# Performance work log

Hardware: AMD Instinct MI355X
Metric: run time of the kernel (lower is better)

## Reference

```python
import jax, jax.numpy as jnp
import numpy as np

FREQ_RES = 100.0 / 256.0
NUM_FILTERS = 6
_CFG = [(0.5, 4.0), (4.0, 8.0), (8.0, 12.0), (12.0, 16.0), (16.0, 24.0), (24.0, 30.0)]
BANDS = [(int(a / FREQ_RES), int(b / FREQ_RES)) for a, b in _CFG]  # (start_bin, end_bin)


def _interp_idx(n_src, n_dst):
    # torch F.interpolate bilinear, align_corners=False, along last dim (T dim is identity since same size)
    j = np.arange(n_dst)
    src = np.maximum((j + 0.5) * n_src / n_dst - 0.5, 0.0)
    x0 = np.floor(src).astype(np.int32)
    x1 = np.minimum(x0 + 1, n_src - 1)
    w = (src - x0).astype(np.float32)
    return x0, x1, w


def _gelu(x):
    return jax.nn.gelu(x, approximate=False)


def _forward(spec, centers, widths, gains, align_w, align_b, fc1_w, fc1_b, fc2_w, fc2_b,
             band_gain, gate_w, gate_b, proj_w, proj_b, bn_gamma, bn_beta, bn_mean, bn_var):
    B, C, T, F = spec.shape
    N = NUM_FILTERS
    band_feats = []
    for i, (s, e) in enumerate(BANDS):
        nb = e - s + 1
        sl = spec[:, :, :, s:e + 1]                       # [B,C,T,nb]
        mu = jax.nn.softplus(centers[i]) + s              # [C,N]
        mu = jnp.clip(mu, s, s + nb - 1)
        std = jnp.clip(jax.nn.softplus(widths[i]) + 1e-3, 0.5, 2.0 * nb / N)
        freqs = jnp.arange(nb, dtype=spec.dtype)          # relative bins [nb]
        g = jnp.exp(-0.5 * ((freqs[None, None, :] - mu[:, :, None]) / std[:, :, None]) ** 2)  # [C,N,nb]
        w = gains[i][:, :, None] * g / (g.sum(-1, keepdims=True) + 1e-6)
        filt = jnp.einsum('bctf,cnf->bctn', sl, w)        # [B,C,T,N]
        aligned = jnp.einsum('bctn,dc->bdtn', filt, align_w[i]) + align_b[i][None, :, None, None]
        band_feats.append(aligned)
    band_stack = jnp.stack(band_feats, axis=1)            # [B,6,C,T,N]
    nb_bands = band_stack.shape[1]
    x = band_stack.reshape(B, nb_bands * C, T, N)
    h = _gelu(jnp.einsum('bktn,ok->botn', x, fc1_w) + fc1_b[None, :, None, None])
    attn = jnp.einsum('botn,ko->bktn', h, fc2_w) + fc2_b[None, :, None, None]
    attn = jax.nn.softmax(attn.reshape(B, nb_bands, C, T, N), axis=1)  # softmax over bands
    band_stack = band_stack * attn * band_gain[None, :, None, None, None]
    enhanced = jnp.zeros_like(spec)
    for i, (s, e) in enumerate(BANDS):
        nb = e - s + 1
        narrow = band_stack[:, i]                         # [B,C,T,N]
        x0, x1, wl = _interp_idx(NUM_FILTERS, nb)
        wl = jnp.asarray(wl, dtype=spec.dtype)
        bf = narrow[..., x0] * (1.0 - wl) + narrow[..., x1] * wl   # [B,C,T,nb]
        enhanced = enhanced.at[:, :, :, s:e + 1].add(bf)
    residual = enhanced - spec
    gate = jax.nn.sigmoid(jnp.einsum('bctf,dc->bdtf', residual, gate_w) + gate_b[None, :, None, None])
    enhanced2 = spec + gate * residual
    y = jnp.einsum('bctf,dc->bdtf', enhanced2, proj_w) + proj_b[None, :, None, None]
    y = (y - bn_mean[None, :, None, None]) / jnp.sqrt(bn_var[None, :, None, None] + 1e-5)
    y = y * bn_gamma[None, :, None, None] + bn_beta[None, :, None, None]
    return _gelu(y)


def setup_inputs() -> dict:
    key = jax.random.key(0)
    ks = jax.random.split(key, 8)
    B, C, T, F, N = 64, 3, 3000, 103, NUM_FILTERS
    spec = jax.random.normal(ks[0], (B, C, T, F), dtype=jnp.float32)
    centers = jnp.stack([jnp.broadcast_to(jnp.linspace(a, b, N, dtype=jnp.float32) / FREQ_RES, (C, N)) for a, b in _CFG])
    widths = jnp.stack([jnp.full((C, N), (b - a) / N / FREQ_RES, dtype=jnp.float32) for a, b in _CFG])
    gains = jnp.ones((6, C, N), jnp.float32)
    align_w = jax.random.normal(ks[1], (6, C, C), dtype=jnp.float32) / np.sqrt(C)
    align_b = jax.random.normal(ks[2], (6, C), dtype=jnp.float32) * 0.02
    inter = 2 * C
    fc1_w = jax.random.normal(ks[3], (inter, 6 * C), dtype=jnp.float32) / np.sqrt(6 * C)
    fc1_b = jnp.zeros((inter,), jnp.float32)
    fc2_w = jax.random.normal(ks[4], (6 * C, inter), dtype=jnp.float32) / np.sqrt(inter)
    fc2_b = jnp.zeros((6 * C,), jnp.float32)
    band_gain = jnp.ones((6,), jnp.float32)
    gate_w = jax.random.normal(ks[5], (C, C), dtype=jnp.float32) / np.sqrt(C)
    gate_b = jnp.zeros((C,), jnp.float32)
    proj_w = jax.random.normal(ks[6], (C, C), dtype=jnp.float32) / np.sqrt(C)
    proj_b = jnp.zeros((C,), jnp.float32)
    bn_gamma = jnp.ones((C,), jnp.float32)
    bn_beta = jnp.zeros((C,), jnp.float32)
    bn_mean = jnp.zeros((C,), jnp.float32)
    bn_var = jnp.ones((C,), jnp.float32)
    return {"spec": spec, "centers": centers, "widths": widths, "gains": gains,
            "align_w": align_w, "align_b": align_b, "fc1_w": fc1_w, "fc1_b": fc1_b,
            "fc2_w": fc2_w, "fc2_b": fc2_b, "band_gain": band_gain,
            "gate_w": gate_w, "gate_b": gate_b, "proj_w": proj_w, "proj_b": proj_b,
            "bn_gamma": bn_gamma, "bn_beta": bn_beta, "bn_mean": bn_mean, "bn_var": bn_var}


def reference(spec, centers, widths, gains, align_w, align_b, fc1_w, fc1_b, fc2_w, fc2_b,
              band_gain, gate_w, gate_b, proj_w, proj_b, bn_gamma, bn_beta, bn_mean, bn_var):
    return _forward(spec, centers, widths, gains, align_w, align_b, fc1_w, fc1_b, fc2_w, fc2_b,
                    band_gain, gate_w, gate_b, proj_w, proj_b, bn_gamma, bn_beta, bn_mean, bn_var)
```

## Files before the change

### kernel.cpp

```cpp
#include <hip/hip_runtime.h>
#include <math.h>

namespace {

constexpr int C_ = 3, T_ = 3000, F_ = 103, NB_ = 6;
constexpr int TT = 12;
constexpr int BS[NB_]  = {1, 10, 20, 30, 40, 61};
constexpr int BNB[NB_] = {10, 11, 11, 11, 22, 16};
constexpr int BOF[NB_] = {0, 10, 21, 32, 43, 65};
constexpr int SPF = 81;
constexpr int PLANE = T_ * F_;
constexpr int SEC = TT * F_;
constexpr int WTOT = 81 * 18;
constexpr int POOLN = C_ * TT * SPF + WTOT;

__device__ __forceinline__ float softplus_full_(float x) {
  return fmaxf(x, 0.0f) + log1pf(expf(-fabsf(x)));
}
__device__ __forceinline__ float sigmoid_(float z) {
  return 1.0f / (1.0f + __expf(-z));
}
__device__ __forceinline__ float gelu_(float x) {
  return x * sigmoid_(1.595769122f * x * (1.0f + 0.044715f * x * x));
}

__global__ __launch_bounds__(128)
void prep_kernel(const float* __restrict__ centers,
                 const float* __restrict__ widths,
                 const float* __restrict__ gains,
                 float* __restrict__ wfilt)
{
  const int q = threadIdx.x;
  if (q >= 108) return;
  int i = q / 18;
  int p = q - i * 18;
  int s = BS[i], nb = BNB[i];
  float mu = softplus_full_(centers[q]) + (float)s;
  mu = fminf(fmaxf(mu, (float)s), (float)(s + nb - 1));
  float sd = softplus_full_(widths[q]) + 0.001f;
  sd = fminf(fmaxf(sd, 0.5f), 2.0f * (float)nb / 6.0f);
  float sum = 0.0f;
  for (int f = 0; f < nb; ++f) {
    float d = ((float)f - mu) / sd;
    sum += __expf(-0.5f * d * d);
  }
  float sc = gains[q] / (sum + 1e-6f);
  float* wrow = &wfilt[BOF[i] * 18 + p * nb];
  for (int f = 0; f < nb; ++f) {
    float d = ((float)f - mu) / sd;
    wrow[f] = sc * __expf(-0.5f * d * d);
  }
}

__global__ __launch_bounds__(256, 6)
void sleepband_kernel(const float* __restrict__ spec,
                      const float* __restrict__ wfilt,
                      const float* __restrict__ align_w,
                      const float* __restrict__ align_b,
                      const float* __restrict__ fc1_w,
                      const float* __restrict__ fc1_b,
                      const float* __restrict__ fc2_w,
                      const float* __restrict__ fc2_b,
                      const float* __restrict__ band_gain,
                      const float* __restrict__ gate_w,
                      const float* __restrict__ gate_b,
                      const float* __restrict__ proj_w,
                      const float* __restrict__ proj_b,
                      const float* __restrict__ bn_gamma,
                      const float* __restrict__ bn_beta,
                      const float* __restrict__ bn_mean,
                      const float* __restrict__ bn_var,
                      float* __restrict__ out)
{
  __shared__ __align__(16) float sPool[POOLN];
  __shared__ float sBand[TT][109];
  __shared__ float sAw[54], sAb[18], sF1[108], sF1b[6], sF2[108], sF2b[18],
                   sBg[6], sGw[9], sGb[3], sPw[9], sPb[3];

  const int tid = threadIdx.x;
  const int t0  = blockIdx.x * TT;
  const int b   = blockIdx.y;

  float* sW = sPool + C_ * TT * SPF;

  const float* specB = spec + (size_t)b * C_ * PLANE;
  for (int li = tid; li < C_ * TT * SPF; li += 256) {
    int c   = li / (TT * SPF);
    int rem = li - c * (TT * SPF);
    int tt  = rem / SPF;
    int f   = rem - tt * SPF;
    sPool[li] = specB[(size_t)c * PLANE + (size_t)(t0 + tt) * F_ + f];
  }
  for (int k = tid; k < WTOT; k += 256) sW[k] = wfilt[k];

  if (tid < 54)  sAw[tid]  = align_w[tid];
  if (tid < 18)  sAb[tid]  = align_b[tid];
  if (tid < 108) sF1[tid]  = fc1_w[tid];
  if (tid < 6)   sF1b[tid] = fc1_b[tid];
  if (tid < 108) sF2[tid]  = fc2_w[tid];
  if (tid < 18)  sF2b[tid] = fc2_b[tid];
  if (tid < 6)   sBg[tid]  = band_gain[tid];
  if (tid < 9)   sGw[tid]  = gate_w[tid];
  if (tid < 3)   sGb[tid]  = gate_b[tid];
  if (tid < 9) {
    int d = tid / 3;
    float sc = bn_gamma[d] * __frsqrt_rn(bn_var[d] + 1e-5f);
    sPw[tid] = proj_w[tid] * sc;
  }
  if (tid < 3) {
    float sc = bn_gamma[tid] * __frsqrt_rn(bn_var[tid] + 1e-5f);
    sPb[tid] = (proj_b[tid] - bn_mean[tid]) * sc + bn_beta[tid];
  }
  __syncthreads();

  if (tid < 18 * TT) {
    int p  = tid / TT;
    int tt = tid - p * TT;
    int c  = p / 6;
    int n  = p - c * 6;
    const float* srowb = &sPool[(c * TT + tt) * SPF];
    #pragma unroll
    for (int i = 0; i < NB_; ++i) {
      const float* wrow = &sW[BOF[i] * 18 + p * BNB[i]];
      const float* srow = srowb + BS[i];
      float acc = 0.0f;
      #pragma unroll
      for (int f = 0; f < BNB[i]; ++f) acc += srow[f] * wrow[f];
      sBand[tt][(i * 3 + c) * 6 + n] = acc;
    }
  }
  __syncthreads();

  if (tid < 6 * TT) {
    int n  = tid / TT;
    int tt = tid - n * TT;
    float al[18];
    #pragma unroll
    for (int i = 0; i < 6; ++i) {
      float f0 = sBand[tt][(i * 3 + 0) * 6 + n];
      float f1 = sBand[tt][(i * 3 + 1) * 6 + n];
      float f2 = sBand[tt][(i * 3 + 2) * 6 + n];
      #pragma unroll
      for (int d = 0; d < 3; ++d)
        al[i * 3 + d] = sAw[i * 9 + d * 3 + 0] * f0 + sAw[i * 9 + d * 3 + 1] * f1 +
                        sAw[i * 9 + d * 3 + 2] * f2 + sAb[i * 3 + d];
    }
    float h[6];
    #pragma unroll
    for (int o = 0; o < 6; ++o) {
      float acc = sF1b[o];
      #pragma unroll
      for (int k = 0; k < 18; ++k) acc += sF1[o * 18 + k] * al[k];
      h[o] = gelu_(acc);
    }
    float at[18];
    #pragma unroll
    for (int k = 0; k < 18; ++k) {
      float acc = sF2b[k];
      #pragma unroll
      for (int o = 0; o < 6; ++o) acc += sF2[k * 6 + o] * h[o];
      at[k] = acc;
    }
    #pragma unroll
    for (int c = 0; c < 3; ++c) {
      float m = at[c];
      #pragma unroll
      for (int i = 1; i < 6; ++i) m = fmaxf(m, at[i * 3 + c]);
      float e[6], ssum = 0.0f;
      #pragma unroll
      for (int i = 0; i < 6; ++i) { e[i] = __expf(at[i * 3 + c] - m); ssum += e[i]; }
      float inv = 1.0f / ssum;
      #pragma unroll
      for (int i = 0; i < 6; ++i)
        sBand[tt][(i * 3 + c) * 6 + n] = al[i * 3 + c] * (e[i] * inv) * sBg[i];
    }
  }
  __syncthreads();

  if (tid < C_ * TT) {
    const int c  = tid / TT;
    const int tt = tid - c * TT;
    float bnd[36];
    #pragma unroll
    for (int i = 0; i < 6; ++i)
      #pragma unroll
      for (int n = 0; n < 6; ++n)
        bnd[i * 6 + n] = sBand[tt][(i * 3 + c) * 6 + n];
    float* row = &sPool[c * SEC + tt * F_];
    row[0] = 0.0f;
    float carry = 0.0f;
    #pragma unroll
    for (int i = 0; i < NB_; ++i) {
      #pragma unroll
      for (int j = 0; j < BNB[i]; ++j) {
        float src = ((float)j + 0.5f) * 6.0f / (float)BNB[i] - 0.5f;
        src = src > 0.0f ? src : 0.0f;
        int   x0 = (int)src;
        int   x1 = (x0 < 5) ? x0 + 1 : 5;
        float wl = src - (float)x0;
        float v  = bnd[i * 6 + x0] * (1.0f - wl) + bnd[i * 6 + x1] * wl;
        if (j == 0) v += carry;
        if (i < NB_ - 1 && j == BNB[i] - 1) carry = v;
        else row[BS[i] + j] = v;
      }
    }
    #pragma unroll
    for (int f = 77; f < F_; ++f) row[f] = 0.0f;
  }
  __syncthreads();

  float gw[9], pw[9], gb3[3], pb3[3];
  #pragma unroll
  for (int k = 0; k < 9; ++k) { gw[k] = sGw[k]; pw[k] = sPw[k]; }
  #pragma unroll
  for (int k = 0; k < 3; ++k) { gb3[k] = sGb[k]; pb3[k] = sPb[k]; }

  const float* sp0 = specB + (size_t)t0 * F_;
  float* outB = out + (size_t)b * C_ * PLANE + (size_t)t0 * F_;
  for (int e4 = tid; e4 < SEC / 4; e4 += 256) {
    const int e = e4 * 4;
    const float4 sA = *(const float4*)(sp0 + e);
    const float4 sB = *(const float4*)(sp0 + PLANE + e);
    const float4 sC = *(const float4*)(sp0 + 2 * PLANE + e);
    const float4 eA = *(const float4*)&sPool[0 * SEC + e];
    const float4 eB = *(const float4*)&sPool[1 * SEC + e];
    const float4 eC = *(const float4*)&sPool[2 * SEC + e];
    float4 oA, oB, oC;
    const float* sAp = (const float*)&sA; const float* sBp = (const float*)&sB;
    const float* sCp = (const float*)&sC;
    const float* eAp = (const float*)&eA; const float* eBp = (const float*)&eB;
    const float* eCp = (const float*)&eC;
    float* oAp = (float*)&oA; float* oBp = (float*)&oB; float* oCp = (float*)&oC;
    #pragma unroll
    for (int j = 0; j < 4; ++j) {
      float sv0 = sAp[j], sv1 = sBp[j], sv2 = sCp[j];
      float r0 = eAp[j] - sv0, r1 = eBp[j] - sv1, r2 = eCp[j] - sv2;
      float e20 = sv0 + sigmoid_(gw[0] * r0 + gw[1] * r1 + gw[2] * r2 + gb3[0]) * r0;
      float e21 = sv1 + sigmoid_(gw[3] * r0 + gw[4] * r1 + gw[5] * r2 + gb3[1]) * r1;
      float e22 = sv2 + sigmoid_(gw[6] * r0 + gw[7] * r1 + gw[8] * r2 + gb3[2]) * r2;
      float y0 = pw[0] * e20 + pw[1] * e21 + pw[2] * e22 + pb3[0];
      float y1 = pw[3] * e20 + pw[4] * e21 + pw[5] * e22 + pb3[1];
      float y2 = pw[6] * e20 + pw[7] * e21 + pw[8] * e22 + pb3[2];
      oAp[j] = gelu_(y0); oBp[j] = gelu_(y1); oCp[j] = gelu_(y2);
    }
    *(float4*)(outB + e) = oA;
    *(float4*)(outB + PLANE + e) = oB;
    *(float4*)(outB + 2 * PLANE + e) = oC;
  }
}

}

extern "C" void kernel_launch(void* const* d_in, const int* in_sizes, int n_in,
                              void* d_out, int out_size, void* d_ws, size_t ws_size,
                              hipStream_t stream) {
  (void)n_in; (void)out_size; (void)ws_size;
  const int B = in_sizes[0] / (C_ * T_ * F_);
  float* wfilt = (float*)d_ws;
  prep_kernel<<<1, 128, 0, stream>>>(
      (const float*)d_in[1], (const float*)d_in[2], (const float*)d_in[3], wfilt);
  dim3 grid(T_ / TT, B);
  sleepband_kernel<<<grid, 256, 0, stream>>>(
      (const float*)d_in[0],  wfilt,
      (const float*)d_in[4],  (const float*)d_in[5],
      (const float*)d_in[6],  (const float*)d_in[7],  (const float*)d_in[8],
      (const float*)d_in[9],  (const float*)d_in[10], (const float*)d_in[11],
      (const float*)d_in[12], (const float*)d_in[13], (const float*)d_in[14],
      (const float*)d_in[15], (const float*)d_in[16], (const float*)d_in[17],
      (const float*)d_in[18], (float*)d_out);
}
```

Baseline: 279.6 us.

## Pad band slots for float4 filter dots, enlarge time tile, hoist BN fold

Spectrum bins are staged into shared memory in a padded per-band slot layout, and filter weights are zero-padded to multiples of four so each band dot product runs as float4 loads. The time tile grows from 12 to 20 rows and the block from 256 to 384 threads. The BN fold into proj weights moves into the prep kernel. Small MLP and gate parameters are now read directly from global memory instead of being staged in shared memory. Larger tiles raise shared memory per block and may cut occupancy, and the direct global reads of uniform weights rely on the cache.

```diff
diff --git a/kernel.cpp b/kernel.cpp
--- a/kernel.cpp
+++ b/kernel.cpp
@@ -4,15 +4,21 @@
 namespace {
 
 constexpr int C_ = 3, T_ = 3000, F_ = 103, NB_ = 6;
-constexpr int TT = 12;
-constexpr int BS[NB_]  = {1, 10, 20, 30, 40, 61};
-constexpr int BNB[NB_] = {10, 11, 11, 11, 22, 16};
-constexpr int BOF[NB_] = {0, 10, 21, 32, 43, 65};
-constexpr int SPF = 81;
+constexpr int TT = 20;
+constexpr int BS_[NB_]  = {1, 10, 20, 30, 40, 61};
+constexpr int BNB_[NB_] = {10, 11, 11, 11, 22, 16};
+constexpr int BP_[NB_]  = {12, 12, 12, 12, 24, 16};
+constexpr int BPS_[NB_] = {0, 12, 24, 36, 48, 72};
+constexpr int WOFP_[NB_] = {0, 216, 432, 648, 864, 1296};
+constexpr int WTOTP = 1584;
+constexpr int SLOTS = 88;
+constexpr int CTSTR = 92;
+constexpr int SPECN = C_ * TT * CTSTR;
 constexpr int PLANE = T_ * F_;
-constexpr int SEC = TT * F_;
-constexpr int WTOT = 81 * 18;
-constexpr int POOLN = C_ * TT * SPF + WTOT;
+constexpr int SEC  = TT * F_;
+constexpr int SECP = 2064;
+constexpr int POOLN = SPECN + WTOTP;
+constexpr int NTHR = 384;
 
 __device__ __forceinline__ float softplus_full_(float x) {
   return fmaxf(x, 0.0f) + log1pf(expf(-fabsf(x)));
@@ -28,33 +34,49 @@
 void prep_kernel(const float* __restrict__ centers,
                  const float* __restrict__ widths,
                  const float* __restrict__ gains,
-                 float* __restrict__ wfilt)
+                 const float* __restrict__ proj_w,
+                 const float* __restrict__ proj_b,
+                 const float* __restrict__ bn_gamma,
+                 const float* __restrict__ bn_beta,
+                 const float* __restrict__ bn_mean,
+                 const float* __restrict__ bn_var,
+                 float* __restrict__ ws)
 {
   const int q = threadIdx.x;
-  if (q >= 108) return;
-  int i = q / 18;
-  int p = q - i * 18;
-  int s = BS[i], nb = BNB[i];
-  float mu = softplus_full_(centers[q]) + (float)s;
-  mu = fminf(fmaxf(mu, (float)s), (float)(s + nb - 1));
-  float sd = softplus_full_(widths[q]) + 0.001f;
-  sd = fminf(fmaxf(sd, 0.5f), 2.0f * (float)nb / 6.0f);
-  float sum = 0.0f;
-  for (int f = 0; f < nb; ++f) {
-    float d = ((float)f - mu) / sd;
-    sum += __expf(-0.5f * d * d);
-  }
-  float sc = gains[q] / (sum + 1e-6f);
-  float* wrow = &wfilt[BOF[i] * 18 + p * nb];
-  for (int f = 0; f < nb; ++f) {
-    float d = ((float)f - mu) / sd;
-    wrow[f] = sc * __expf(-0.5f * d * d);
-  }
-}
-
-__global__ __launch_bounds__(256, 6)
+  if (q < 108) {
+    int i = q / 18;
+    int p = q - i * 18;
+    int s = BS_[i], nb = BNB_[i];
+    float mu = softplus_full_(centers[q]) + (float)s;
+    mu = fminf(fmaxf(mu, (float)s), (float)(s + nb - 1));
+    float sd = softplus_full_(widths[q]) + 0.001f;
+    sd = fminf(fmaxf(sd, 0.5f), 2.0f * (float)nb / 6.0f);
+    float sum = 0.0f;
+    for (int f = 0; f < nb; ++f) {
+      float d = ((float)f - mu) / sd;
+      sum += __expf(-0.5f * d * d);
+    }
+    float sc = gains[q] / (sum + 1e-6f);
+    float* wrow = &ws[WOFP_[i] + p * BP_[i]];
+    for (int f = 0; f < nb; ++f) {
+      float d = ((float)f - mu) / sd;
+      wrow[f] = sc * __expf(-0.5f * d * d);
+    }
+    for (int f = nb; f < BP_[i]; ++f) wrow[f] = 0.0f;
+  } else if (q < 117) {
+    int k = q - 108, d = k / 3;
+    float sc = bn_gamma[d] / sqrtf(bn_var[d] + 1e-5f);
+    ws[WTOTP + k] = proj_w[k] * sc;
+  } else if (q < 120) {
+    int d = q - 117;
+    float sc = bn_gamma[d] / sqrtf(bn_var[d] + 1e-5f);
+    ws[WTOTP + 9 + d] = (proj_b[d] - bn_mean[d]) * sc + bn_beta[d];
+  }
+}
+
+__global__ __launch_bounds__(NTHR, 6)
 void sleepband_kernel(const float* __restrict__ spec,
-                      const float* __restrict__ wfilt,
+                      const float* __restrict__ ws,
                       const float* __restrict__ align_w,
                       const float* __restrict__ align_b,
                       const float* __restrict__ fc1_w,
@@ -64,76 +86,57 @@
                       const float* __restrict__ band_gain,
                       const float* __restrict__ gate_w,
                       const float* __restrict__ gate_b,
-                      const float* __restrict__ proj_w,
-                      const float* __restrict__ proj_b,
-                      const float* __restrict__ bn_gamma,
-                      const float* __restrict__ bn_beta,
-                      const float* __restrict__ bn_mean,
-                      const float* __restrict__ bn_var,
                       float* __restrict__ out)
 {
   __shared__ __align__(16) float sPool[POOLN];
   __shared__ float sBand[TT][109];
-  __shared__ float sAw[54], sAb[18], sF1[108], sF1b[6], sF2[108], sF2b[18],
-                   sBg[6], sGw[9], sGb[3], sPw[9], sPb[3];
 
   const int tid = threadIdx.x;
   const int t0  = blockIdx.x * TT;
   const int b   = blockIdx.y;
-
-  float* sW = sPool + C_ * TT * SPF;
-
   const float* specB = spec + (size_t)b * C_ * PLANE;
-  for (int li = tid; li < C_ * TT * SPF; li += 256) {
-    int c   = li / (TT * SPF);
-    int rem = li - c * (TT * SPF);
-    int tt  = rem / SPF;
-    int f   = rem - tt * SPF;
-    sPool[li] = specB[(size_t)c * PLANE + (size_t)(t0 + tt) * F_ + f];
-  }
-  for (int k = tid; k < WTOT; k += 256) sW[k] = wfilt[k];
-
-  if (tid < 54)  sAw[tid]  = align_w[tid];
-  if (tid < 18)  sAb[tid]  = align_b[tid];
-  if (tid < 108) sF1[tid]  = fc1_w[tid];
-  if (tid < 6)   sF1b[tid] = fc1_b[tid];
-  if (tid < 108) sF2[tid]  = fc2_w[tid];
-  if (tid < 18)  sF2b[tid] = fc2_b[tid];
-  if (tid < 6)   sBg[tid]  = band_gain[tid];
-  if (tid < 9)   sGw[tid]  = gate_w[tid];
-  if (tid < 3)   sGb[tid]  = gate_b[tid];
-  if (tid < 9) {
-    int d = tid / 3;
-    float sc = bn_gamma[d] * __frsqrt_rn(bn_var[d] + 1e-5f);
-    sPw[tid] = proj_w[tid] * sc;
-  }
-  if (tid < 3) {
-    float sc = bn_gamma[tid] * __frsqrt_rn(bn_var[tid] + 1e-5f);
-    sPb[tid] = (proj_b[tid] - bn_mean[tid]) * sc + bn_beta[tid];
-  }
+
+  for (int li = tid; li < C_ * TT * SLOTS; li += NTHR) {
+    int ctt  = li / SLOTS;
+    int slot = li - ctt * SLOTS;
+    int c    = ctt / TT;
+    int tt   = ctt - c * TT;
+    int i    = (slot >= 72) ? 5 : ((slot >= 48) ? 4 : (slot / 12));
+    int j    = slot - BPS_[i];
+    float v  = 0.0f;
+    if (j < BNB_[i])
+      v = specB[(size_t)c * PLANE + (size_t)(t0 + tt) * F_ + (BS_[i] + j)];
+    sPool[ctt * CTSTR + slot] = v;
+  }
+  for (int k = tid; k < WTOTP; k += NTHR) sPool[SPECN + k] = ws[k];
   __syncthreads();
 
   if (tid < 18 * TT) {
-    int p  = tid / TT;
-    int tt = tid - p * TT;
-    int c  = p / 6;
-    int n  = p - c * 6;
-    const float* srowb = &sPool[(c * TT + tt) * SPF];
+    const int p  = tid / TT;
+    const int tt = tid - p * TT;
+    const int c  = p / 6;
+    const int n  = p - c * 6;
+    const float* srow = &sPool[(c * TT + tt) * CTSTR];
+    const float* wall = &sPool[SPECN];
     #pragma unroll
     for (int i = 0; i < NB_; ++i) {
-      const float* wrow = &sW[BOF[i] * 18 + p * BNB[i]];
-      const float* srow = srowb + BS[i];
-      float acc = 0.0f;
-      #pragma unroll
-      for (int f = 0; f < BNB[i]; ++f) acc += srow[f] * wrow[f];
-      sBand[tt][(i * 3 + c) * 6 + n] = acc;
+      const float4* s4 = (const float4*)(srow + BPS_[i]);
+      const float4* w4 = (const float4*)(wall + WOFP_[i] + p * BP_[i]);
+      float4 a = {0.0f, 0.0f, 0.0f, 0.0f};
+      #pragma unroll
+      for (int k = 0; k < BP_[i] / 4; ++k) {
+        float4 sv = s4[k], wv = w4[k];
+        a.x += sv.x * wv.x; a.y += sv.y * wv.y;
+        a.z += sv.z * wv.z; a.w += sv.w * wv.w;
+      }
+      sBand[tt][(i * 3 + c) * 6 + n] = (a.x + a.y) + (a.z + a.w);
     }
   }
   __syncthreads();
 
   if (tid < 6 * TT) {
-    int n  = tid / TT;
-    int tt = tid - n * TT;
+    const int n  = tid / TT;
+    const int tt = tid - n * TT;
     float al[18];
     #pragma unroll
     for (int i = 0; i < 6; ++i) {
@@ -142,23 +145,23 @@
       float f2 = sBand[tt][(i * 3 + 2) * 6 + n];
       #pragma unroll
       for (int d = 0; d < 3; ++d)
-        al[i * 3 + d] = sAw[i * 9 + d * 3 + 0] * f0 + sAw[i * 9 + d * 3 + 1] * f1 +
-                        sAw[i * 9 + d * 3 + 2] * f2 + sAb[i * 3 + d];
+        al[i * 3 + d] = align_w[i * 9 + d * 3 + 0] * f0 + align_w[i * 9 + d * 3 + 1] * f1 +
+                        align_w[i * 9 + d * 3 + 2] * f2 + align_b[i * 3 + d];
     }
     float h[6];
     #pragma unroll
     for (int o = 0; o < 6; ++o) {
-      float acc = sF1b[o];
-      #pragma unroll
-      for (int k = 0; k < 18; ++k) acc += sF1[o * 18 + k] * al[k];
+      float acc = fc1_b[o];
+      #pragma unroll
+      for (int k = 0; k < 18; ++k) acc += fc1_w[o * 18 + k] * al[k];
       h[o] = gelu_(acc);
     }
     float at[18];
     #pragma unroll
     for (int k = 0; k < 18; ++k) {
-      float acc = sF2b[k];
-      #pragma unroll
-      for (int o = 0; o < 6; ++o) acc += sF2[k * 6 + o] * h[o];
+      float acc = fc2_b[k];
+      #pragma unroll
+      for (int o = 0; o < 6; ++o) acc += fc2_w[k * 6 + o] * h[o];
       at[k] = acc;
     }
     #pragma unroll
@@ -172,7 +175,7 @@
       float inv = 1.0f / ssum;
       #pragma unroll
       for (int i = 0; i < 6; ++i)
-        sBand[tt][(i * 3 + c) * 6 + n] = al[i * 3 + c] * (e[i] * inv) * sBg[i];
+        sBand[tt][(i * 3 + c) * 6 + n] = al[i * 3 + c] * (e[i] * inv) * band_gain[i];
     }
   }
   __syncthreads();
@@ -186,22 +189,22 @@
       #pragma unroll
       for (int n = 0; n < 6; ++n)
         bnd[i * 6 + n] = sBand[tt][(i * 3 + c) * 6 + n];
-    float* row = &sPool[c * SEC + tt * F_];
+    float* row = &sPool[c * SECP + tt * F_];
     row[0] = 0.0f;
     float carry = 0.0f;
     #pragma unroll
     for (int i = 0; i < NB_; ++i) {
       #pragma unroll
-      for (int j = 0; j < BNB[i]; ++j) {
-        float src = ((float)j + 0.5f) * 6.0f / (float)BNB[i] - 0.5f;
+      for (int j = 0; j < BNB_[i]; ++j) {
+        float src = ((float)j + 0.5f) * 6.0f / (float)BNB_[i] - 0.5f;
         src = src > 0.0f ? src : 0.0f;
         int   x0 = (int)src;
         int   x1 = (x0 < 5) ? x0 + 1 : 5;
         float wl = src - (float)x0;
         float v  = bnd[i * 6 + x0] * (1.0f - wl) + bnd[i * 6 + x1] * wl;
         if (j == 0) v += carry;
-        if (i < NB_ - 1 && j == BNB[i] - 1) carry = v;
-        else row[BS[i] + j] = v;
+        if (i < NB_ - 1 && j == BNB_[i] - 1) carry = v;
+        else row[BS_[i] + j] = v;
       }
     }
     #pragma unroll
@@ -211,20 +214,20 @@
 
   float gw[9], pw[9], gb3[3], pb3[3];
   #pragma unroll
-  for (int k = 0; k < 9; ++k) { gw[k] = sGw[k]; pw[k] = sPw[k]; }
+  for (int k = 0; k < 9; ++k) { gw[k] = gate_w[k]; pw[k] = ws[WTOTP + k]; }
   #pragma unroll
-  for (int k = 0; k < 3; ++k) { gb3[k] = sGb[k]; pb3[k] = sPb[k]; }
+  for (int k = 0; k < 3; ++k) { gb3[k] = gate_b[k]; pb3[k] = ws[WTOTP + 9 + k]; }
 
   const float* sp0 = specB + (size_t)t0 * F_;
   float* outB = out + (size_t)b * C_ * PLANE + (size_t)t0 * F_;
-  for (int e4 = tid; e4 < SEC / 4; e4 += 256) {
+  for (int e4 = tid; e4 < SEC / 4; e4 += NTHR) {
     const int e = e4 * 4;
     const float4 sA = *(const float4*)(sp0 + e);
     const float4 sB = *(const float4*)(sp0 + PLANE + e);
     const float4 sC = *(const float4*)(sp0 + 2 * PLANE + e);
-    const float4 eA = *(const float4*)&sPool[0 * SEC + e];
-    const float4 eB = *(const float4*)&sPool[1 * SEC + e];
-    const float4 eC = *(const float4*)&sPool[2 * SEC + e];
+    const float4 eA = *(const float4*)&sPool[0 * SECP + e];
+    const float4 eB = *(const float4*)&sPool[1 * SECP + e];
+    const float4 eC = *(const float4*)&sPool[2 * SECP + e];
     float4 oA, oB, oC;
     const float* sAp = (const float*)&sA; const float* sBp = (const float*)&sB;
     const float* sCp = (const float*)&sC;
@@ -256,16 +259,16 @@
                               hipStream_t stream) {
   (void)n_in; (void)out_size; (void)ws_size;
   const int B = in_sizes[0] / (C_ * T_ * F_);
-  float* wfilt = (float*)d_ws;
+  float* ws = (float*)d_ws;
   prep_kernel<<<1, 128, 0, stream>>>(
-      (const float*)d_in[1], (const float*)d_in[2], (const float*)d_in[3], wfilt);
+      (const float*)d_in[1],  (const float*)d_in[2],  (const float*)d_in[3],
+      (const float*)d_in[13], (const float*)d_in[14], (const float*)d_in[15],
+      (const float*)d_in[16], (const float*)d_in[17], (const float*)d_in[18], ws);
   dim3 grid(T_ / TT, B);
-  sleepband_kernel<<<grid, 256, 0, stream>>>(
-      (const float*)d_in[0],  wfilt,
+  sleepband_kernel<<<grid, NTHR, 0, stream>>>(
+      (const float*)d_in[0],  ws,
       (const float*)d_in[4],  (const float*)d_in[5],
       (const float*)d_in[6],  (const float*)d_in[7],  (const float*)d_in[8],
       (const float*)d_in[9],  (const float*)d_in[10], (const float*)d_in[11],
-      (const float*)d_in[12], (const float*)d_in[13], (const float*)d_in[14],
-      (const float*)d_in[15], (const float*)d_in[16], (const float*)d_in[17],
-      (const float*)d_in[18], (float*)d_out);
-}
+      (const float*)d_in[12], (float*)d_out);
+}
```

Result: slower. 449.9 us (+60.9%).
